# Kernel tuning notes

Hardware: AMD Instinct MI355X
Metric: run time of the kernel (lower is better)

The kernel has to match this reference:

```python
import jax, jax.numpy as jnp
import numpy as np

N_NODES = 50000
N_EDGES = 200000
D_IN = 512
D_OUT = 512

def setup_inputs() -> dict:
    key = jax.random.key(0)
    k1, k2, k3, k4, k5, k6 = jax.random.split(key, 6)
    h = jax.random.normal(k1, (N_NODES, D_IN), dtype=jnp.float32)
    W = jax.random.normal(k2, (D_IN, D_OUT), dtype=jnp.float32) * (1.0 / np.sqrt(D_IN))
    b = jax.random.normal(k3, (D_OUT,), dtype=jnp.float32) * 0.01
    edge_weight = jax.random.uniform(k4, (N_EDGES,), dtype=jnp.float32)
    src = jax.random.randint(k5, (N_EDGES,), 0, N_NODES, dtype=jnp.int32)
    dst = jax.random.randint(k6, (N_EDGES,), 0, N_NODES, dtype=jnp.int32)
    return {"h": h, "W": W, "b": b, "edge_weight": edge_weight, "src": src, "dst": dst}

def reference(h, W, b, edge_weight, src, dst):
    # Linear projection of source-node features (nn.Linear)
    h_proj = h @ W + b                                   # [N, D_OUT]
    # u_mul_e: gather projected src features, scale by scalar edge weight
    msg = h_proj[src] * edge_weight[:, None]             # [E, D_OUT]
    # mean aggregation over incoming edges per destination node (DGL fn.mean)
    sums = jax.ops.segment_sum(msg, dst, num_segments=N_NODES)          # [N, D_OUT]
    cnt = jax.ops.segment_sum(jnp.ones_like(edge_weight), dst, num_segments=N_NODES)  # [N]
    agg = sums / jnp.maximum(cnt, 1.0)[:, None]          # zero-in-degree nodes -> 0
    # ReLU then dropout (eval mode -> identity)
    return jax.nn.relu(agg)
```

## Files before the change

kernel.cpp:

```cpp
#include <hip/hip_runtime.h>

#define NNODES 50000
#define NEDGES 200000
#define DDIM 512

typedef __attribute__((ext_vector_type(8))) short bf16x8;
typedef __attribute__((ext_vector_type(4))) float f32x4;

static __device__ __forceinline__ unsigned short f2bf(float f) {
  unsigned u = __float_as_uint(f);
  unsigned r = (u + 0x7fffu + ((u >> 16) & 1u)) >> 16;
  return (unsigned short)r;
}

static __device__ __forceinline__ void gload_lds16(const void* g, void* l) {
  __builtin_amdgcn_global_load_lds(
      (const __attribute__((address_space(1))) unsigned int*)g,
      (__attribute__((address_space(3))) unsigned int*)l, 16, 0, 0);
}

static __device__ __forceinline__ bf16x8 cvt_frag(f32x4 lo, f32x4 hi) {
  union { bf16x8 v; unsigned u[4]; } r;
  asm("v_cvt_pk_bf16_f32 %0, %1, %2" : "=v"(r.u[0]) : "v"(lo.x), "v"(lo.y));
  asm("v_cvt_pk_bf16_f32 %0, %1, %2" : "=v"(r.u[1]) : "v"(lo.z), "v"(lo.w));
  asm("v_cvt_pk_bf16_f32 %0, %1, %2" : "=v"(r.u[2]) : "v"(hi.x), "v"(hi.y));
  asm("v_cvt_pk_bf16_f32 %0, %1, %2" : "=v"(r.u[3]) : "v"(hi.z), "v"(hi.w));
  return r.v;
}

__global__ __launch_bounds__(256) void cvt_wt_kernel(
    const float* __restrict__ W, unsigned short* __restrict__ Wt,
    int* __restrict__ deg) {
  const int gid = (blockIdx.x + blockIdx.y * gridDim.x) * 256 + threadIdx.x;
  if (gid < NNODES) deg[gid] = 0;

  __shared__ float t[32][33];
  const int n0 = blockIdx.x * 32, k0 = blockIdx.y * 32;
  const int tx = threadIdx.x & 31, ty = threadIdx.x >> 5;
  for (int r = ty; r < 32; r += 8)
    t[r][tx] = W[(size_t)(k0 + r) * DDIM + n0 + tx];
  __syncthreads();
  for (int r = ty; r < 32; r += 8)
    Wt[(size_t)(n0 + r) * DDIM + k0 + tx] = f2bf(t[tx][r]);
}

__global__ __launch_bounds__(256) void gemm_mfma_kernel(
    const float* __restrict__ A, const unsigned short* __restrict__ Bt,
    const float* __restrict__ bias, unsigned short* __restrict__ C, int M) {
  __shared__ float Af[2][128 * 32];
  __shared__ unsigned short Bs[2][128 * 32];
  const int tid = threadIdx.x;
  const int wid = tid >> 6, lane = tid & 63;

  const int nwg = gridDim.x;
  const int q = nwg >> 3, rr = nwg & 7;
  const int x = blockIdx.x & 7, idx = blockIdx.x >> 3;
  const int wg = x * q + min(x, rr) + idx;

  const int mt = wg >> 2, nt = wg & 3;
  const int bm = mt * 128, bn = nt * 128;

  f32x4 acc[2][8] = {};

  const int lr = lane >> 3;
  const int kqs = (lane & 7) ^ lr;
  const int ar0 = min(bm + 0 * 32 + wid * 8 + lr, M - 1);
  const int ar1 = min(bm + 1 * 32 + wid * 8 + lr, M - 1);
  const int ar2 = min(bm + 2 * 32 + wid * 8 + lr, M - 1);
  const int ar3 = min(bm + 3 * 32 + wid * 8 + lr, M - 1);
  const float* pa0 = A + (size_t)ar0 * DDIM + kqs * 4;
  const float* pa1 = A + (size_t)ar1 * DDIM + kqs * 4;
  const float* pa2 = A + (size_t)ar2 * DDIM + kqs * 4;
  const float* pa3 = A + (size_t)ar3 * DDIM + kqs * 4;

  const int r0 = tid >> 2;
  const int cge = (tid & 3) ^ ((r0 >> 1) & 3);
  const unsigned short* b0 = Bt + (size_t)(bn + r0) * DDIM + cge * 8;
  const unsigned short* b1 = Bt + (size_t)(bn + r0 + 64) * DDIM + cge * 8;

  const int l16 = lane & 15, lk = lane >> 4;
  const int lke = lk ^ ((l16 >> 1) & 3);
  const int s7 = l16 & 7;

  const int sOff0 = (wid * 64) * 8;
  const int sOff1 = (256 + wid * 64) * 8;

#define STAGE(buf, k0)                                   \
  do {                                                   \
    gload_lds16(pa0 + (k0), &Af[buf][wid * 256]);        \
    gload_lds16(pa1 + (k0), &Af[buf][1024 + wid * 256]); \
    gload_lds16(pa2 + (k0), &Af[buf][2048 + wid * 256]); \
    gload_lds16(pa3 + (k0), &Af[buf][3072 + wid * 256]); \
    gload_lds16(b0 + (k0), &Bs[buf][sOff0]);             \
    gload_lds16(b1 + (k0), &Bs[buf][sOff1]);             \
  } while (0)

#define COMPUTE(buf)                                                          \
  do {                                                                        \
    bf16x8 af[2], bfr[8];                                                     \
    _Pragma("unroll") for (int i = 0; i < 2; ++i) {                           \
      const int rowi = (wid * 32 + i * 16 + l16) * 32;                        \
      const f32x4 lo = *(const f32x4*)&Af[buf][rowi + (((2 * lk) ^ s7) << 2)];\
      const f32x4 hi = *(const f32x4*)&Af[buf][rowi + (((2 * lk + 1) ^ s7) << 2)]; \
      af[i] = cvt_frag(lo, hi);                                               \
    }                                                                         \
    _Pragma("unroll") for (int j = 0; j < 8; ++j)                             \
      bfr[j] = *(const bf16x8*)&Bs[buf][(j * 16 + l16) * 32 + lke * 8];       \
    _Pragma("unroll") for (int i = 0; i < 2; ++i)                             \
        _Pragma("unroll") for (int j = 0; j < 8; ++j)                         \
            acc[i][j] = __builtin_amdgcn_mfma_f32_16x16x32_bf16(              \
                af[i], bfr[j], acc[i][j], 0, 0, 0);                           \
  } while (0)

  STAGE(0, 0);
  __syncthreads();
#pragma unroll 2
  for (int t = 0; t < 15; ++t) {
    const int cur = t & 1;
    STAGE(cur ^ 1, (t + 1) * 32);
    COMPUTE(cur);
    __syncthreads();
  }
  COMPUTE(1);
  __syncthreads();

  unsigned short* cl = (unsigned short*)&Af[0][0] + wid * 4096;
#pragma unroll
  for (int j = 0; j < 8; ++j) {
    const float bv = bias[bn + j * 16 + l16];
#pragma unroll
    for (int i = 0; i < 2; ++i)
#pragma unroll
      for (int qq = 0; qq < 4; ++qq)
        cl[(i * 16 + lk * 4 + qq) * 128 + j * 16 + l16] =
            f2bf(acc[i][j][qq] + bv);
  }
  __syncthreads();
#pragma unroll
  for (int pass = 0; pass < 8; ++pass) {
    const int rt = pass * 4 + (lane >> 4);
    const int c0 = (lane & 15) * 8;
    const int grow = bm + wid * 32 + rt;
    if (grow < M) {
      const uint4 v = *(const uint4*)&cl[rt * 128 + c0];
      *(uint4*)&C[(size_t)grow * DDIM + bn + c0] = v;
    }
  }
#undef STAGE
#undef COMPUTE
}

__global__ __launch_bounds__(256) void hist_kernel(const int* __restrict__ dst,
                                                   int* __restrict__ deg, int E) {
  const int e = blockIdx.x * 256 + threadIdx.x;
  if (e < E) atomicAdd(&deg[dst[e]], 1);
}

__global__ __launch_bounds__(256) void chunk_sum_kernel(
    const int* __restrict__ deg, int* __restrict__ part, int n) {
  const int base = blockIdx.x * 1024;
  int v = 0;
  for (int i = threadIdx.x; i < 1024; i += 256) {
    const int idx = base + i;
    v += (idx < n) ? deg[idx] : 0;
  }
#pragma unroll
  for (int s = 32; s; s >>= 1) v += __shfl_down(v, s, 64);
  __shared__ int ws[4];
  if ((threadIdx.x & 63) == 0) ws[threadIdx.x >> 6] = v;
  __syncthreads();
  if (threadIdx.x == 0) part[blockIdx.x] = ws[0] + ws[1] + ws[2] + ws[3];
}

__global__ void scan_part_kernel(int* __restrict__ part, int nb) {
  const int lane = threadIdx.x & 63;
  int v = (lane < nb) ? part[lane] : 0;
  int incl = v;
#pragma unroll
  for (int s = 1; s < 64; s <<= 1) {
    int t = __shfl_up(incl, s, 64);
    if (lane >= s) incl += t;
  }
  if (lane < nb) part[lane] = incl - v;
}

__global__ __launch_bounds__(1024) void chunk_scan_kernel(
    const int* __restrict__ deg, const int* __restrict__ part,
    int* __restrict__ off, int* __restrict__ cur, int n) {
  __shared__ int wsum[16];
  const int tid = threadIdx.x, lane = tid & 63, wid = tid >> 6;
  const int i = blockIdx.x * 1024 + tid;
  const int v = (i < n) ? deg[i] : 0;
  int incl = v;
#pragma unroll
  for (int s = 1; s < 64; s <<= 1) {
    int t = __shfl_up(incl, s, 64);
    if (lane >= s) incl += t;
  }
  if (lane == 63) wsum[wid] = incl;
  __syncthreads();
  if (wid == 0 && lane < 16) {
    int wv = wsum[lane];
#pragma unroll
    for (int s = 1; s < 16; s <<= 1) {
      int t = __shfl_up(wv, s, 16);
      if (lane >= s) wv += t;
    }
    wsum[lane] = wv;
  }
  __syncthreads();
  const int add = part[blockIdx.x] + ((wid > 0) ? wsum[wid - 1] : 0);
  if (i < n) {
    off[i + 1] = add + incl;
    cur[i] = add + incl - v;
  }
  if (i == 0) off[0] = 0;
}

__global__ __launch_bounds__(256) void fill_kernel(
    const int* __restrict__ src, const int* __restrict__ dst,
    const float* __restrict__ ew, int* __restrict__ cur,
    uint2* __restrict__ epair, int E) {
  const int e = blockIdx.x * 256 + threadIdx.x;
  if (e >= E) return;
  const int p = atomicAdd(&cur[dst[e]], 1);
  epair[p] = make_uint2((unsigned)src[e], __float_as_uint(ew[e]));
}

__global__ __launch_bounds__(256) void gather_kernel(
    const unsigned short* __restrict__ hp, const int* __restrict__ off,
    const uint2* __restrict__ epair, float* __restrict__ out, int n) {
  const int node = blockIdx.x * 4 + (threadIdx.x >> 6);
  if (node >= n) return;
  const int lane = threadIdx.x & 63;
  const int beg = off[node], end = off[node + 1];

  float acc[8] = {0.f, 0.f, 0.f, 0.f, 0.f, 0.f, 0.f, 0.f};
  int p = beg;
  for (; p + 4 <= end; p += 4) {
    uint2 e[4];
    uint4 u[4];
#pragma unroll
    for (int m = 0; m < 4; ++m) e[m] = epair[p + m];
#pragma unroll
    for (int m = 0; m < 4; ++m)
      u[m] = *(const uint4*)(hp + (size_t)e[m].x * DDIM + lane * 8);
#pragma unroll
    for (int m = 0; m < 4; ++m) {
      const float w = __uint_as_float(e[m].y);
      const unsigned a[4] = {u[m].x, u[m].y, u[m].z, u[m].w};
#pragma unroll
      for (int qv = 0; qv < 4; ++qv) {
        acc[2 * qv + 0] += w * __uint_as_float(a[qv] << 16);
        acc[2 * qv + 1] += w * __uint_as_float(a[qv] & 0xffff0000u);
      }
    }
  }
  for (; p < end; ++p) {
    const uint2 e0 = epair[p];
    const float w0 = __uint_as_float(e0.y);
    const uint4 u0 = *(const uint4*)(hp + (size_t)e0.x * DDIM + lane * 8);
    const unsigned a0[4] = {u0.x, u0.y, u0.z, u0.w};
#pragma unroll
    for (int qv = 0; qv < 4; ++qv) {
      acc[2 * qv + 0] += w0 * __uint_as_float(a0[qv] << 16);
      acc[2 * qv + 1] += w0 * __uint_as_float(a0[qv] & 0xffff0000u);
    }
  }

  const float inv = 1.0f / fmaxf((float)(end - beg), 1.0f);
  f32x4 o0, o1;
  o0.x = fmaxf(acc[0] * inv, 0.f);
  o0.y = fmaxf(acc[1] * inv, 0.f);
  o0.z = fmaxf(acc[2] * inv, 0.f);
  o0.w = fmaxf(acc[3] * inv, 0.f);
  o1.x = fmaxf(acc[4] * inv, 0.f);
  o1.y = fmaxf(acc[5] * inv, 0.f);
  o1.z = fmaxf(acc[6] * inv, 0.f);
  o1.w = fmaxf(acc[7] * inv, 0.f);
  float* orow = out + (size_t)node * DDIM + lane * 8;
  __builtin_nontemporal_store(o0, (f32x4*)(orow + 0));
  __builtin_nontemporal_store(o1, (f32x4*)(orow + 4));
}

extern "C" void kernel_launch(void* const* d_in, const int* in_sizes, int n_in,
                              void* d_out, int out_size, void* d_ws, size_t ws_size,
                              hipStream_t stream) {
  const float* h  = (const float*)d_in[0];
  const float* W  = (const float*)d_in[1];
  const float* b  = (const float*)d_in[2];
  const float* ew = (const float*)d_in[3];
  const int* src  = (const int*)d_in[4];
  const int* dst  = (const int*)d_in[5];
  float* out = (float*)d_out;

  char* ws = (char*)d_ws;
  size_t o = 0;
  auto alloc = [&](size_t bytes) {
    char* p = ws + o;
    o += (bytes + 255) & ~(size_t)255;
    return p;
  };
  unsigned short* hp = (unsigned short*)alloc((size_t)NNODES * DDIM * 2);
  unsigned short* Wt = (unsigned short*)alloc((size_t)DDIM * DDIM * 2);
  int* deg    = (int*)alloc((size_t)NNODES * 4);
  int* off    = (int*)alloc((size_t)(NNODES + 1) * 4);
  int* cur    = (int*)alloc((size_t)NNODES * 4);
  uint2* epair = (uint2*)alloc((size_t)NEDGES * 8);
  int* part   = (int*)alloc(64 * 4);

  const int nchunks = (NNODES + 1023) / 1024;

  dim3 wgrid(16, 16);
  cvt_wt_kernel<<<wgrid, 256, 0, stream>>>(W, Wt, deg);

  const int mtiles = (NNODES + 127) / 128;
  gemm_mfma_kernel<<<mtiles * 4, 256, 0, stream>>>(h, Wt, b, hp, NNODES);

  hist_kernel<<<(NEDGES + 255) / 256, 256, 0, stream>>>(dst, deg, NEDGES);
  chunk_sum_kernel<<<nchunks, 256, 0, stream>>>(deg, part, NNODES);
  scan_part_kernel<<<1, 64, 0, stream>>>(part, nchunks);
  chunk_scan_kernel<<<nchunks, 1024, 0, stream>>>(deg, part, off, cur, NNODES);
  fill_kernel<<<(NEDGES + 255) / 256, 256, 0, stream>>>(src, dst, ew, cur,
                                                        epair, NEDGES);

  gather_kernel<<<(NNODES + 3) / 4, 256, 0, stream>>>(hp, off, epair, out,
                                                      NNODES);
}
```

Baseline: 148.5 us.

## Preload full-K bf16 A slab in LDS and retile GEMM to 48x256

The GEMM now loads a 48-row strip of A for the whole K dimension once, converts it to bf16 and keeps it in a swizzled LDS slab. Only B tiles are double-buffered per K step, and each wave owns a 64-column slice of a 256-wide N tile. This removes the repeated fp32 A staging and per-step conversions, and halves how often A is re-read across N tiles (2 instead of 4). The cost is a larger LDS footprint, a synchronous A prologue with no overlap, and smaller per-wave MFMA tiles.

Result: slower. 157.6 us (+6.1%).

```diff
diff --git a/kernel.cpp b/kernel.cpp
--- a/kernel.cpp
+++ b/kernel.cpp
@@ -47,106 +47,114 @@
 __global__ __launch_bounds__(256) void gemm_mfma_kernel(
     const float* __restrict__ A, const unsigned short* __restrict__ Bt,
     const float* __restrict__ bias, unsigned short* __restrict__ C, int M) {
-  __shared__ float Af[2][128 * 32];
-  __shared__ unsigned short Bs[2][128 * 32];
+  __shared__ unsigned short Aslab[48 * 512];
+  __shared__ unsigned short Bs[2][256 * 32];
   const int tid = threadIdx.x;
   const int wid = tid >> 6, lane = tid & 63;
 
   const int nwg = gridDim.x;
-  const int q = nwg >> 3, rr = nwg & 7;
+  const int q = nwg >> 3, rr8 = nwg & 7;
   const int x = blockIdx.x & 7, idx = blockIdx.x >> 3;
-  const int wg = x * q + min(x, rr) + idx;
-
-  const int mt = wg >> 2, nt = wg & 3;
-  const int bm = mt * 128, bn = nt * 128;
-
-  f32x4 acc[2][8] = {};
-
-  const int lr = lane >> 3;
-  const int kqs = (lane & 7) ^ lr;
-  const int ar0 = min(bm + 0 * 32 + wid * 8 + lr, M - 1);
-  const int ar1 = min(bm + 1 * 32 + wid * 8 + lr, M - 1);
-  const int ar2 = min(bm + 2 * 32 + wid * 8 + lr, M - 1);
-  const int ar3 = min(bm + 3 * 32 + wid * 8 + lr, M - 1);
-  const float* pa0 = A + (size_t)ar0 * DDIM + kqs * 4;
-  const float* pa1 = A + (size_t)ar1 * DDIM + kqs * 4;
-  const float* pa2 = A + (size_t)ar2 * DDIM + kqs * 4;
-  const float* pa3 = A + (size_t)ar3 * DDIM + kqs * 4;
-
-  const int r0 = tid >> 2;
-  const int cge = (tid & 3) ^ ((r0 >> 1) & 3);
-  const unsigned short* b0 = Bt + (size_t)(bn + r0) * DDIM + cge * 8;
-  const unsigned short* b1 = Bt + (size_t)(bn + r0 + 64) * DDIM + cge * 8;
+  const int wg = x * q + min(x, rr8) + idx;
+
+  const int mt = wg >> 1, nt = wg & 1;
+  const int bm = mt * 48, bn = nt * 256;
+
+  f32x4 acc[3][4] = {};
 
   const int l16 = lane & 15, lk = lane >> 4;
   const int lke = lk ^ ((l16 >> 1) & 3);
-  const int s7 = l16 & 7;
-
-  const int sOff0 = (wid * 64) * 8;
-  const int sOff1 = (256 + wid * 64) * 8;
-
-#define STAGE(buf, k0)                                   \
-  do {                                                   \
-    gload_lds16(pa0 + (k0), &Af[buf][wid * 256]);        \
-    gload_lds16(pa1 + (k0), &Af[buf][1024 + wid * 256]); \
-    gload_lds16(pa2 + (k0), &Af[buf][2048 + wid * 256]); \
-    gload_lds16(pa3 + (k0), &Af[buf][3072 + wid * 256]); \
-    gload_lds16(b0 + (k0), &Bs[buf][sOff0]);             \
-    gload_lds16(b1 + (k0), &Bs[buf][sOff1]);             \
+
+  {
+    const int prow = tid >> 4;
+    const int pcol = (tid & 15) * 32;
+#pragma unroll
+    for (int rr = 0; rr < 3; ++rr) {
+      const int row = rr * 16 + prow;
+      const int grow = min(bm + row, M - 1);
+      const float* src = A + (size_t)grow * DDIM + pcol;
+      f32x4 v[8];
+#pragma unroll
+      for (int qv = 0; qv < 8; ++qv) v[qv] = ((const f32x4*)src)[qv];
+#pragma unroll
+      for (int q2 = 0; q2 < 4; ++q2) {
+        const bf16x8 w = cvt_frag(v[2 * q2], v[2 * q2 + 1]);
+        const int c = (pcol >> 3) + q2;
+        *(bf16x8*)&Aslab[row * 512 + (c ^ (row & 7)) * 8] = w;
+      }
+    }
+  }
+
+  const unsigned short* pb[4];
+  int dstOff[4];
+#pragma unroll
+  for (int p = 0; p < 4; ++p) {
+    const int sidx = p * 256 + tid;
+    const int brow = sidx >> 2;
+    const int cg = (sidx & 3) ^ ((brow >> 1) & 3);
+    pb[p] = Bt + (size_t)(bn + brow) * DDIM + cg * 8;
+    dstOff[p] = sidx * 8;
+  }
+
+#define BSTAGE(buf, k0)                                       \
+  do {                                                        \
+    gload_lds16(pb[0] + (k0), &Bs[buf][(0 * 256 + wid * 64) * 8]); \
+    gload_lds16(pb[1] + (k0), &Bs[buf][(1 * 256 + wid * 64) * 8]); \
+    gload_lds16(pb[2] + (k0), &Bs[buf][(2 * 256 + wid * 64) * 8]); \
+    gload_lds16(pb[3] + (k0), &Bs[buf][(3 * 256 + wid * 64) * 8]); \
   } while (0)
 
-#define COMPUTE(buf)                                                          \
+#define COMPUTE(buf, step)                                                    \
   do {                                                                        \
-    bf16x8 af[2], bfr[8];                                                     \
-    _Pragma("unroll") for (int i = 0; i < 2; ++i) {                           \
-      const int rowi = (wid * 32 + i * 16 + l16) * 32;                        \
-      const f32x4 lo = *(const f32x4*)&Af[buf][rowi + (((2 * lk) ^ s7) << 2)];\
-      const f32x4 hi = *(const f32x4*)&Af[buf][rowi + (((2 * lk + 1) ^ s7) << 2)]; \
-      af[i] = cvt_frag(lo, hi);                                               \
+    bf16x8 af[3], bfr[4];                                                     \
+    _Pragma("unroll") for (int i = 0; i < 3; ++i) {                           \
+      const int row = i * 16 + l16;                                           \
+      const int c = (step) * 4 + lk;                                          \
+      af[i] = *(const bf16x8*)&Aslab[row * 512 + (c ^ (row & 7)) * 8];        \
     }                                                                         \
-    _Pragma("unroll") for (int j = 0; j < 8; ++j)                             \
-      bfr[j] = *(const bf16x8*)&Bs[buf][(j * 16 + l16) * 32 + lke * 8];       \
-    _Pragma("unroll") for (int i = 0; i < 2; ++i)                             \
-        _Pragma("unroll") for (int j = 0; j < 8; ++j)                         \
+    _Pragma("unroll") for (int j = 0; j < 4; ++j)                             \
+      bfr[j] = *(const bf16x8*)&Bs[buf][(wid * 64 + j * 16 + l16) * 32 + lke * 8]; \
+    _Pragma("unroll") for (int i = 0; i < 3; ++i)                             \
+        _Pragma("unroll") for (int j = 0; j < 4; ++j)                         \
             acc[i][j] = __builtin_amdgcn_mfma_f32_16x16x32_bf16(              \
                 af[i], bfr[j], acc[i][j], 0, 0, 0);                           \
   } while (0)
 
-  STAGE(0, 0);
+  BSTAGE(0, 0);
   __syncthreads();
 #pragma unroll 2
   for (int t = 0; t < 15; ++t) {
     const int cur = t & 1;
-    STAGE(cur ^ 1, (t + 1) * 32);
-    COMPUTE(cur);
+    BSTAGE(cur ^ 1, (t + 1) * 32);
+    COMPUTE(cur, t);
     __syncthreads();
   }
-  COMPUTE(1);
-  __syncthreads();
-
-  unsigned short* cl = (unsigned short*)&Af[0][0] + wid * 4096;
-#pragma unroll
-  for (int j = 0; j < 8; ++j) {
-    const float bv = bias[bn + j * 16 + l16];
-#pragma unroll
-    for (int i = 0; i < 2; ++i)
+  COMPUTE(1, 15);
+  __syncthreads();
+
+  unsigned short* cl = &Bs[0][0] + wid * 3072;
+#pragma unroll
+  for (int j = 0; j < 4; ++j) {
+    const float bv = bias[bn + wid * 64 + j * 16 + l16];
+#pragma unroll
+    for (int i = 0; i < 3; ++i)
 #pragma unroll
       for (int qq = 0; qq < 4; ++qq)
-        cl[(i * 16 + lk * 4 + qq) * 128 + j * 16 + l16] =
+        cl[(i * 16 + lk * 4 + qq) * 64 + j * 16 + l16] =
             f2bf(acc[i][j][qq] + bv);
   }
   __syncthreads();
 #pragma unroll
-  for (int pass = 0; pass < 8; ++pass) {
-    const int rt = pass * 4 + (lane >> 4);
-    const int c0 = (lane & 15) * 8;
-    const int grow = bm + wid * 32 + rt;
+  for (int pass = 0; pass < 6; ++pass) {
+    const int rt = pass * 8 + (lane >> 3);
+    const int c0 = (lane & 7) * 8;
+    const int grow = bm + rt;
     if (grow < M) {
-      const uint4 v = *(const uint4*)&cl[rt * 128 + c0];
-      *(uint4*)&C[(size_t)grow * DDIM + bn + c0] = v;
-    }
-  }
-#undef STAGE
+      const uint4 v = *(const uint4*)&cl[rt * 64 + c0];
+      *(uint4*)&C[(size_t)grow * DDIM + bn + wid * 64 + c0] = v;
+    }
+  }
+#undef BSTAGE
 #undef COMPUTE
 }
 
@@ -314,8 +322,8 @@
   dim3 wgrid(16, 16);
   cvt_wt_kernel<<<wgrid, 256, 0, stream>>>(W, Wt, deg);
 
-  const int mtiles = (NNODES + 127) / 128;
-  gemm_mfma_kernel<<<mtiles * 4, 256, 0, stream>>>(h, Wt, b, hp, NNODES);
+  const int nmt = (NNODES + 47) / 48;
+  gemm_mfma_kernel<<<nmt * 2, 256, 0, stream>>>(h, Wt, b, hp, NNODES);
 
   hist_kernel<<<(NEDGES + 255) / 256, 256, 0, stream>>>(dst, deg, NEDGES);
   chunk_sum_kernel<<<nchunks, 256, 0, stream>>>(deg, part, NNODES);
```
